# Kernel tuning notes

Measured on AMD Instinct MI355X. Metric: run time of the kernel, lower is better.

## Reference

```python
import jax, jax.numpy as jnp
import numpy as np

B, S, D, H, HG, W, DFF = 2, 4096, 1024, 16, 2, 128, 4096
NEG = -1e30  # stands in for -inf in the original masking (exp underflows to exactly 0)


def _chunk(x, w):
    # overlapping chunks of size 2w with hop w (tf.signal.frame equivalent)
    b, s, d = x.shape
    blocks = x.reshape(b, s // w, w, d)
    return jnp.concatenate([blocks[:, :-1], blocks[:, 1:]], axis=2)  # [b, s//w-1, 2w, d]


def _sliding_scores(q, k, w):
    # q,k: [BH, S, dh] (q pre-scaled). Returns banded scores [BH, S, 2w+1].
    bh, s, d = q.shape
    c = s // w - 1
    attn = jnp.einsum('bcxd,bcyd->bcxy', _chunk(q, w), _chunk(k, w))  # [bh,c,2w,2w]
    # pad one row then reshape: the skew trick from the source (_pad_and_transpose_last_two_dims)
    dca = jnp.pad(attn, ((0, 0), (0, 0), (0, 1), (0, 0))).reshape(bh, c, 2 * w, 2 * w + 1)
    up = jnp.concatenate([dca[:, :, :w, :w + 1], dca[:, -1:, w:, :w + 1]], axis=1)          # [bh,c+1,w,w+1]
    first = jnp.roll(dca, shift=(1, w), axis=(2, 3))[:, :1, :w, :w]                          # first-chunk lower triangle
    low = jnp.concatenate([first, dca[:, :, -(w + 1):-1, w + 1:]], axis=1)                   # [bh,c+1,w,w]
    return jnp.concatenate([low, up], axis=-1).reshape(bh, s, 2 * w + 1)


def _invalid_mask(s, w):
    # _mask_invalid_locations: mask band positions that fall outside [0, S)
    m = jnp.tril(jnp.ones((w, w + 1), jnp.float32))[::-1]
    m = jnp.pad(m, ((0, s - w), (0, w)))
    return (m + m[::-1, ::-1]) > 0  # [s, 2w+1]


def _sliding_value(p, v, w):
    # p: [BH, S, 2w+1] band probs, v: [BH, S, dh] -> [BH, S, dh]
    bh, s, kk = p.shape
    d = v.shape[-1]
    c = s // w
    cp = jnp.pad(p.reshape(bh, c, w, kk), ((0, 0), (0, 0), (0, 0), (0, w + 1)))
    # pad-and-diagonalize skew: row r shifted right by r -> aligns band with 3w value window
    cp = cp.reshape(bh, c, w * (3 * w + 2))[:, :, :-w].reshape(bh, c, w, 3 * w + 1)[:, :, :, :-1]
    pv = jnp.pad(v, ((0, 0), (w, w), (0, 0))).reshape(bh, c + 2, w, d)
    cv = jnp.concatenate([pv[:, :-2], pv[:, 1:-1], pv[:, 2:]], axis=2)  # [bh,c,3w,d]
    return jnp.einsum('bcwk,bckd->bcwd', cp, cv).reshape(bh, s, d)


def _layernorm(x, g, b):
    mu = jnp.mean(x, -1, keepdims=True)
    var = jnp.mean(jnp.square(x - mu), -1, keepdims=True)
    return (x - mu) * jax.lax.rsqrt(var + 1e-6) * g + b


def setup_inputs() -> dict:
    key = jax.random.key(0)
    ks = jax.random.split(key, 8)
    dense = lambda k, i, o: 0.02 * jax.random.normal(k, (i, o), jnp.float32)
    return {
        'x': jax.random.normal(ks[0], (B, S, D), jnp.float32),
        'mask': jnp.zeros((B, 1, 1, S), jnp.float32),
        'wq_k': dense(ks[1], D, D), 'wq_b': jnp.zeros((D,), jnp.float32),
        'wk_k': dense(ks[2], D, D), 'wk_b': jnp.zeros((D,), jnp.float32),
        'wv_k': dense(ks[3], D, D), 'wv_b': jnp.zeros((D,), jnp.float32),
        'wo_k': dense(ks[4], D, D), 'wo_b': jnp.zeros((D,), jnp.float32),
        'ffn_w1': dense(ks[5], D, DFF), 'ffn_b1': jnp.zeros((DFF,), jnp.float32),
        'ffn_w2': dense(ks[6], DFF, D), 'ffn_b2': jnp.zeros((D,), jnp.float32),
        'ln1_g': jnp.ones((D,), jnp.float32), 'ln1_b': jnp.zeros((D,), jnp.float32),
        'ln2_g': jnp.ones((D,), jnp.float32), 'ln2_b': jnp.zeros((D,), jnp.float32),
    }


def reference(x, mask, wq_k, wq_b, wk_k, wk_b, wv_k, wv_b, wo_k, wo_b,
              ffn_w1, ffn_b1, ffn_w2, ffn_b2, ln1_g, ln1_b, ln2_g, ln2_b):
    dh = D // H
    hl = H - HG
    split = lambda t: t.reshape(B, S, H, dh).transpose(0, 2, 1, 3)  # [B,H,S,dh]
    q, k, v = split(x @ wq_k + wq_b), split(x @ wk_k + wk_b), split(x @ wv_k + wv_b)
    scale = 1.0 / jnp.sqrt(jnp.float32(dh))
    # ---- local (sliding-window) heads ----
    ql = (q[:, :hl] * scale).reshape(B * hl, S, dh)
    kl = k[:, :hl].reshape(B * hl, S, dh)
    vl = v[:, :hl].reshape(B * hl, S, dh)
    scores = _sliding_scores(ql, kl, W)
    scores = jnp.where(_invalid_mask(S, W)[None], NEG, scores)
    out_l = _sliding_value(jax.nn.softmax(scores, axis=-1), vl, W).reshape(B, hl, S, dh)
    # ---- global heads (full attention, graph_mask=None branch) ----
    logits = jnp.einsum('bhqd,bhkd->bhqk', q[:, hl:], k[:, hl:]) * scale + mask * (-1000.0)
    out_g = jnp.einsum('bhqk,bhkd->bhqd', jax.nn.softmax(logits, axis=-1), v[:, hl:])
    # ---- merge heads, output proj, residual + LN, FFN (leaky_relu alpha=0.2 = tf default) ----
    attn = jnp.concatenate([out_l, out_g], axis=1).transpose(0, 2, 1, 3).reshape(B, S, D)
    out1 = _layernorm(x + attn @ wo_k + wo_b, ln1_g, ln1_b)
    h = jax.nn.leaky_relu(out1 @ ffn_w1 + ffn_b1, negative_slope=0.2)
    return _layernorm(out1 + h @ ffn_w2 + ffn_b2, ln2_g, ln2_b)
```

## Files before the change

### kernel.cpp

```cpp
#include <hip/hip_runtime.h>
#include <hip/hip_bf16.h>

typedef unsigned short u16;
typedef unsigned int u32;
typedef __attribute__((ext_vector_type(8))) short short8;
typedef __attribute__((ext_vector_type(8))) unsigned short ushort8v;
typedef __attribute__((ext_vector_type(4))) unsigned short ushort4v;
typedef __attribute__((ext_vector_type(4))) float f32x4;

static constexpr int B_ = 2, S_ = 4096, D_ = 1024, H_ = 16, HG_ = 2, W_ = 128, DFF_ = 4096;
static constexpr int HL_ = H_ - HG_;
static constexpr int M_ = B_ * S_;
static constexpr int NCH_ = 4;

static __device__ __forceinline__ u16 f2b(float f) {
    u32 u = __builtin_bit_cast(u32, f);
    u32 r = (u + 0x7fffu + ((u >> 16) & 1u)) >> 16;
    return (u16)r;
}
static __device__ __forceinline__ float b2f(u16 b) {
    return __builtin_bit_cast(float, (u32)b << 16);
}

__global__ __launch_bounds__(256) void k_f32_to_bf16(const float* __restrict__ src,
                                                     u16* __restrict__ dst, int n4) {
    int i = blockIdx.x * 256 + threadIdx.x;
    if (i >= n4) return;
    float4 v = reinterpret_cast<const float4*>(src)[i];
    ushort4v o; o[0] = f2b(v.x); o[1] = f2b(v.y); o[2] = f2b(v.z); o[3] = f2b(v.w);
    reinterpret_cast<ushort4v*>(dst)[i] = o;
}

__global__ __launch_bounds__(256) void k_transpose_bf16(const float* __restrict__ src,
                                                        u16* __restrict__ dst,
                                                        int K, int N, int ro) {
    __shared__ float tile[32][33];
    const int tx = threadIdx.x & 31, ty = threadIdx.x >> 5;
    const int bx = blockIdx.x, by = blockIdx.y;
#pragma unroll
    for (int jj = 0; jj < 4; ++jj) {
        int kk = by * 32 + ty + jj * 8;
        int nn = bx * 32 + tx;
        tile[ty + jj * 8][tx] = src[(size_t)kk * N + nn];
    }
    __syncthreads();
#pragma unroll
    for (int jj = 0; jj < 4; ++jj) {
        int nn = bx * 32 + ty + jj * 8;
        int kk = by * 32 + tx;
        dst[(size_t)(ro + nn) * K + kk] = f2b(tile[tx][ty + jj * 8]);
    }
}

__global__ __launch_bounds__(256) void k_transpose_v(const u16* __restrict__ qkv,
                                                     u16* __restrict__ vT) {
    __shared__ u16 tile[32][33];
    const int tx = threadIdx.x & 31, ty = threadIdx.x >> 5;
    const int s0 = blockIdx.x * 32;
    const int d0 = blockIdx.y * 32;
    const int bh = blockIdx.z;
    const int b = bh >> 4, h = bh & 15;
#pragma unroll
    for (int jj = 0; jj < 4; ++jj) {
        int srow = s0 + ty + jj * 8;
        tile[ty + jj * 8][tx] = qkv[(size_t)(b * S_ + srow) * 3072 + 2048 + h * 64 + d0 + tx];
    }
    __syncthreads();
#pragma unroll
    for (int jj = 0; jj < 4; ++jj) {
        int d = d0 + ty + jj * 8;
        vT[(size_t)((b * H_ + h) * 64 + d) * S_ + s0 + tx] = tile[tx][ty + jj * 8];
    }
}

__global__ void k_pack_bias3(const float* __restrict__ a, const float* __restrict__ b,
                             const float* __restrict__ c, float* __restrict__ dst) {
    int i = blockIdx.x * 256 + threadIdx.x;
    if (i >= 3072) return;
    dst[i] = i < 1024 ? a[i] : (i < 2048 ? b[i - 1024] : c[i - 2048]);
}

#define GLDS16(gp, lp) __builtin_amdgcn_global_load_lds( \
    (const __attribute__((address_space(1))) void*)(gp),  \
    (__attribute__((address_space(3))) void*)(lp), 16, 0, 0)

template <int N>
static __device__ __forceinline__ void vwait() {
    if constexpr (N == 0) asm volatile("s_waitcnt vmcnt(0)" ::: "memory");
    else if constexpr (N == 3) asm volatile("s_waitcnt vmcnt(3)" ::: "memory");
    else asm volatile("s_waitcnt vmcnt(4)" ::: "memory");
    __builtin_amdgcn_sched_barrier(0);
}

template <int BM, bool LEAKY, bool OUTF, bool OUTB>
__global__ __launch_bounds__(512, 2) void k_gemm8(const u16* __restrict__ A, const u16* __restrict__ Bt,
                                                  const float* __restrict__ bias,
                                                  float* __restrict__ Cf, u16* __restrict__ Cb,
                                                  int M, int N, int K) {
    constexpr int MR = BM / 32;
    constexpr int LA = BM / 128;
    constexpr int AHALF = BM * 64;
    constexpr int ABUF = 2 * AHALF;
    constexpr int BHALF = 16384;
    constexpr int PARSZ = ABUF + 2 * BHALF;
    constexpr int NWT = LA + 2;

    __shared__ __align__(16) char smem[2 * PARSZ];

    const int tid = threadIdx.x;
    const int lane = tid & 63, w = tid >> 6;
    const int wm = w >> 2, wn = w & 3;
    const int c = lane & 15, g = lane >> 4;

    const int GX = gridDim.x;
    const int nwg = GX * gridDim.y;
    const int lin = blockIdx.y * GX + blockIdx.x;
    const int qq = nwg >> 3, rm = nwg & 7;
    const int xcd = lin & 7, idx = lin >> 3;
    const int wg = (xcd < rm ? xcd * (qq + 1) : rm * (qq + 1) + (xcd - rm) * qq) + idx;
    const int m0 = (wg % GX) * BM;
    const int n0 = (wg / GX) * 256;

    const int srr = lane >> 2;
    const int sgc = (lane & 3) ^ ((lane >> 4) & 2);
    const u16* gA0 = A + (size_t)(m0 + w * 16 + srr) * K + sgc * 8;
    const u16* gA1 = (LA == 2) ? (A + (size_t)(m0 + 128 + w * 16 + srr) * K + sgc * 8) : gA0;
    const u16* gB0 = Bt + (size_t)(n0 + w * 16 + srr) * K + sgc * 8;
    const u16* gB1 = Bt + (size_t)(n0 + 128 + w * 16 + srr) * K + sgc * 8;

#define STG_A(par, kh, kt) do { \
        char* _d = smem + (par) * PARSZ + (kh) * AHALF + w * 1024; \
        GLDS16(gA0 + (size_t)(kt) * 64 + (kh) * 32, _d); \
        if (LA == 2) GLDS16(gA1 + (size_t)(kt) * 64 + (kh) * 32, _d + 8192); \
    } while (0)
#define STG_B(par, kh, kt) do { \
        char* _d = smem + (par) * PARSZ + ABUF + (kh) * BHALF + w * 1024; \
        GLDS16(gB0 + (size_t)(kt) * 64 + (kh) * 32, _d); \
        GLDS16(gB1 + (size_t)(kt) * 64 + (kh) * 32, _d + 8192); \
    } while (0)

    const int gb = (g ^ ((c >> 3) << 1)) * 16;
    const int arow = c * 64 + gb;

    f32x4 acc[MR][4];
#pragma unroll
    for (int i = 0; i < MR; ++i)
#pragma unroll
        for (int j = 0; j < 4; ++j)
#pragma unroll
            for (int e = 0; e < 4; ++e) acc[i][j][e] = 0.f;

    STG_A(0, 0, 0); STG_B(0, 0, 0); STG_A(0, 1, 0); STG_B(0, 1, 0);
    vwait<0>();
    __builtin_amdgcn_s_barrier();

    const int NK = K >> 6;
    short8 af[MR], b0, b1;
    for (int kt = 0; kt < NK; ++kt) {
        const int par = kt & 1, nxt = par ^ 1;
        const char* bp = smem + par * PARSZ;
        const bool more = (kt + 1) < NK;
#pragma unroll
        for (int mi = 0; mi < MR; ++mi)
            af[mi] = *reinterpret_cast<const short8*>(bp + (wm * MR + mi) * 1024 + arow);
        b0 = *reinterpret_cast<const short8*>(bp + ABUF + (wn * 4 + 0) * 1024 + arow);
        b1 = *reinterpret_cast<const short8*>(bp + ABUF + (wn * 4 + 1) * 1024 + arow);
        if (more) STG_A(nxt, 0, kt + 1);
        __builtin_amdgcn_s_barrier();
        __builtin_amdgcn_s_setprio(1);
#pragma unroll
        for (int mi = 0; mi < MR; ++mi) {
            acc[mi][0] = __builtin_amdgcn_mfma_f32_16x16x32_bf16(af[mi], b0, acc[mi][0], 0, 0, 0);
            acc[mi][1] = __builtin_amdgcn_mfma_f32_16x16x32_bf16(af[mi], b1, acc[mi][1], 0, 0, 0);
        }
        __builtin_amdgcn_s_setprio(0);
        __builtin_amdgcn_s_barrier();
        b0 = *reinterpret_cast<const short8*>(bp + ABUF + (wn * 4 + 2) * 1024 + arow);
        b1 = *reinterpret_cast<const short8*>(bp + ABUF + (wn * 4 + 3) * 1024 + arow);
        if (more) STG_B(nxt, 0, kt + 1);
        __builtin_amdgcn_s_barrier();
        __builtin_amdgcn_s_setprio(1);
#pragma unroll
        for (int mi = 0; mi < MR; ++mi) {
            acc[mi][2] = __builtin_amdgcn_mfma_f32_16x16x32_bf16(af[mi], b0, acc[mi][2], 0, 0, 0);
            acc[mi][3] = __builtin_amdgcn_mfma_f32_16x16x32_bf16(af[mi], b1, acc[mi][3], 0, 0, 0);
        }
        __builtin_amdgcn_s_setprio(0);
        if (more) vwait<NWT>(); else vwait<0>();
        __builtin_amdgcn_s_barrier();
#pragma unroll
        for (int mi = 0; mi < MR; ++mi)
            af[mi] = *reinterpret_cast<const short8*>(bp + AHALF + (wm * MR + mi) * 1024 + arow);
        b0 = *reinterpret_cast<const short8*>(bp + ABUF + BHALF + (wn * 4 + 0) * 1024 + arow);
        b1 = *reinterpret_cast<const short8*>(bp + ABUF + BHALF + (wn * 4 + 1) * 1024 + arow);
        if (more) STG_A(nxt, 1, kt + 1);
        __builtin_amdgcn_s_barrier();
        __builtin_amdgcn_s_setprio(1);
#pragma unroll
        for (int mi = 0; mi < MR; ++mi) {
            acc[mi][0] = __builtin_amdgcn_mfma_f32_16x16x32_bf16(af[mi], b0, acc[mi][0], 0, 0, 0);
            acc[mi][1] = __builtin_amdgcn_mfma_f32_16x16x32_bf16(af[mi], b1, acc[mi][1], 0, 0, 0);
        }
        __builtin_amdgcn_s_setprio(0);
        __builtin_amdgcn_s_barrier();
        b0 = *reinterpret_cast<const short8*>(bp + ABUF + BHALF + (wn * 4 + 2) * 1024 + arow);
        b1 = *reinterpret_cast<const short8*>(bp + ABUF + BHALF + (wn * 4 + 3) * 1024 + arow);
        if (more) STG_B(nxt, 1, kt + 1);
        __builtin_amdgcn_s_barrier();
        __builtin_amdgcn_s_setprio(1);
#pragma unroll
        for (int mi = 0; mi < MR; ++mi) {
            acc[mi][2] = __builtin_amdgcn_mfma_f32_16x16x32_bf16(af[mi], b0, acc[mi][2], 0, 0, 0);
            acc[mi][3] = __builtin_amdgcn_mfma_f32_16x16x32_bf16(af[mi], b1, acc[mi][3], 0, 0, 0);
        }
        __builtin_amdgcn_s_setprio(0);
        if (more) vwait<NWT>();
        __builtin_amdgcn_s_barrier();
    }

#pragma unroll
    for (int mi = 0; mi < MR; ++mi) {
        const int rowb = m0 + wm * (BM / 2) + mi * 16 + g * 4;
#pragma unroll
        for (int ni = 0; ni < 4; ++ni) {
            const int col = n0 + wn * 64 + ni * 16 + c;
            const float bs = bias[col];
#pragma unroll
            for (int j = 0; j < 4; ++j) {
                float v = acc[mi][ni][j] + bs;
                if (LEAKY) v = v > 0.f ? v : 0.2f * v;
                const size_t idxo = (size_t)(rowb + j) * N + col;
                if (OUTF) Cf[idxo] = v;
                if (OUTB) Cb[idxo] = f2b(v);
            }
        }
    }
#undef STG_A
#undef STG_B
}

__global__ __launch_bounds__(256) void k_attn_local(const u16* __restrict__ qkv,
                                                    const u16* __restrict__ vT,
                                                    u16* __restrict__ out) {
    __shared__ __align__(16) u16 Kl[64][72];
    __shared__ __align__(16) u16 Vl[64][72];
    __shared__ __align__(16) u16 Pl[4][1024];
    const int tid = threadIdx.x, lane = tid & 63, wave = tid >> 6;
    const int c = lane & 15, g = lane >> 4;
    const int b = blockIdx.z, h = blockIdx.y;
    const int q0 = blockIdx.x * 64;
    const int qrow = q0 + wave * 16 + c;

    short8 qf[2];
    {
        const u16* qp = qkv + (size_t)(b * S_ + qrow) * 3072 + h * 64 + g * 8;
        qf[0] = *reinterpret_cast<const short8*>(qp);
        qf[1] = *reinterpret_cast<const short8*>(qp + 32);
    }

    f32x4 acc[4];
#pragma unroll
    for (int dt = 0; dt < 4; ++dt)
#pragma unroll
        for (int j = 0; j < 4; ++j) acc[dt][j] = 0.f;
    float mrow = -1e30f, lrow = 0.f;

    const int t_lo = max(0, q0 - W_) >> 6;
    const int t_hi = min(S_ - 1, q0 + 63 + W_) >> 6;
    u16* pw = Pl[wave];

    for (int t = t_lo; t <= t_hi; ++t) {
        __syncthreads();
#pragma unroll
        for (int it = 0; it < 2; ++it) {
            int L = it * 256 + tid;
            int r = L >> 3, cb = (L & 7) * 8;
            *reinterpret_cast<ushort8v*>(&Kl[r][cb]) =
                *reinterpret_cast<const ushort8v*>(&qkv[(size_t)(b * S_ + t * 64 + r) * 3072 + 1024 + h * 64 + cb]);
            *reinterpret_cast<ushort8v*>(&Vl[r][cb]) =
                *reinterpret_cast<const ushort8v*>(&vT[(size_t)((b * H_ + h) * 64 + r) * S_ + t * 64 + cb]);
        }
        __syncthreads();

        f32x4 s[4];
#pragma unroll
        for (int nt = 0; nt < 4; ++nt)
#pragma unroll
            for (int j = 0; j < 4; ++j) s[nt][j] = 0.f;
        __builtin_amdgcn_s_setprio(1);
#pragma unroll
        for (int kc = 0; kc < 2; ++kc) {
#pragma unroll
            for (int nt = 0; nt < 4; ++nt) {
                short8 kf = *reinterpret_cast<const short8*>(&Kl[nt * 16 + c][kc * 32 + g * 8]);
                s[nt] = __builtin_amdgcn_mfma_f32_16x16x32_bf16(kf, qf[kc], s[nt], 0, 0, 0);
            }
        }
        __builtin_amdgcn_s_setprio(0);

        float p[4][4];
        float tmax = -1e30f;
#pragma unroll
        for (int nt = 0; nt < 4; ++nt)
#pragma unroll
            for (int j = 0; j < 4; ++j) {
                float sv = s[nt][j] * 0.125f;
                int key = t * 64 + nt * 16 + 4 * g + j;
                bool val = (key >= qrow - W_) && (key <= qrow + W_);
                sv = val ? sv : -1e30f;
                p[nt][j] = sv;
                tmax = fmaxf(tmax, sv);
            }
        tmax = fmaxf(tmax, __shfl_xor(tmax, 16));
        tmax = fmaxf(tmax, __shfl_xor(tmax, 32));
        float mnew = fmaxf(mrow, tmax);
        float fac = __expf(mrow - mnew);
        mrow = mnew;
        float psum = 0.f;
#pragma unroll
        for (int nt = 0; nt < 4; ++nt)
#pragma unroll
            for (int j = 0; j < 4; ++j) {
                p[nt][j] = __expf(p[nt][j] - mnew);
                psum += p[nt][j];
            }
        lrow = lrow * fac + psum;
#pragma unroll
        for (int dt = 0; dt < 4; ++dt)
#pragma unroll
            for (int j = 0; j < 4; ++j) acc[dt][j] *= fac;

#pragma unroll
        for (int nt = 0; nt < 4; ++nt)
#pragma unroll
            for (int jp = 0; jp < 2; ++jp) {
                u32 pk = (u32)f2b(p[nt][2 * jp]) | ((u32)f2b(p[nt][2 * jp + 1]) << 16);
                int byteoff = (c << 7) + ((nt * 32 + 8 * g + 4 * jp) ^ ((c & 7) << 4));
                *reinterpret_cast<u32*>(reinterpret_cast<char*>(pw) + byteoff) = pk;
            }
        asm volatile("s_waitcnt lgkmcnt(0)" ::: "memory");

        __builtin_amdgcn_s_setprio(1);
#pragma unroll
        for (int h2 = 0; h2 < 2; ++h2) {
            int rb = (c << 7) + ((h2 * 64 + g * 16) ^ ((c & 7) << 4));
            short8 pa = *reinterpret_cast<const short8*>(reinterpret_cast<char*>(pw) + rb);
#pragma unroll
            for (int dt = 0; dt < 4; ++dt) {
                short8 vf = *reinterpret_cast<const short8*>(&Vl[dt * 16 + c][h2 * 32 + g * 8]);
                acc[dt] = __builtin_amdgcn_mfma_f32_16x16x32_bf16(vf, pa, acc[dt], 0, 0, 0);
            }
        }
        __builtin_amdgcn_s_setprio(0);
    }

    float lfull = lrow + __shfl_xor(lrow, 16);
    lfull += __shfl_xor(lfull, 32);
    const float rinv = 1.0f / lfull;

#pragma unroll
    for (int dt = 0; dt < 4; ++dt) {
        u32 w0 = (u32)f2b(acc[dt][0] * rinv) | ((u32)f2b(acc[dt][1] * rinv) << 16);
        u32 w1 = (u32)f2b(acc[dt][2] * rinv) | ((u32)f2b(acc[dt][3] * rinv) << 16);
        uint2 wv; wv.x = w0; wv.y = w1;
        *reinterpret_cast<uint2*>(out + (size_t)(b * S_ + qrow) * 1024 + h * 64 + dt * 16 + 4 * g) = wv;
    }
}

__global__ __launch_bounds__(256) void k_attn_global_part(const u16* __restrict__ qkv,
                                                          const u16* __restrict__ vT,
                                                          const float* __restrict__ mask,
                                                          float* __restrict__ po,
                                                          float* __restrict__ ml) {
    __shared__ __align__(16) u16 Kl[64][72];
    __shared__ __align__(16) u16 Vl[64][72];
    __shared__ __align__(16) u16 Pl[4][1024];
    __shared__ float maskl[64];
    const int tid = threadIdx.x, lane = tid & 63, wave = tid >> 6;
    const int c = lane & 15, g = lane >> 4;
    const int b = blockIdx.z;
    const int hh = blockIdx.y >> 2, ch = blockIdx.y & 3;
    const int h = HL_ + hh;
    const int q0 = blockIdx.x * 64;
    const int qrow = q0 + wave * 16 + c;

    short8 qf[2];
    {
        const u16* qp = qkv + (size_t)(b * S_ + qrow) * 3072 + h * 64 + g * 8;
        qf[0] = *reinterpret_cast<const short8*>(qp);
        qf[1] = *reinterpret_cast<const short8*>(qp + 32);
    }

    f32x4 acc[4];
#pragma unroll
    for (int dt = 0; dt < 4; ++dt)
#pragma unroll
        for (int j = 0; j < 4; ++j) acc[dt][j] = 0.f;
    float mrow = -1e30f, lrow = 0.f;
    u16* pw = Pl[wave];

    const int t_lo = ch * (S_ / 64 / NCH_), t_hi = t_lo + (S_ / 64 / NCH_) - 1;
    for (int t = t_lo; t <= t_hi; ++t) {
        __syncthreads();
#pragma unroll
        for (int it = 0; it < 2; ++it) {
            int L = it * 256 + tid;
            int r = L >> 3, cb = (L & 7) * 8;
            *reinterpret_cast<ushort8v*>(&Kl[r][cb]) =
                *reinterpret_cast<const ushort8v*>(&qkv[(size_t)(b * S_ + t * 64 + r) * 3072 + 1024 + h * 64 + cb]);
            *reinterpret_cast<ushort8v*>(&Vl[r][cb]) =
                *reinterpret_cast<const ushort8v*>(&vT[(size_t)((b * H_ + h) * 64 + r) * S_ + t * 64 + cb]);
        }
        if (tid < 64) maskl[tid] = mask[b * S_ + t * 64 + tid] * (-1000.0f);
        __syncthreads();

        f32x4 s[4];
#pragma unroll
        for (int nt = 0; nt < 4; ++nt)
#pragma unroll
            for (int j = 0; j < 4; ++j) s[nt][j] = 0.f;
        __builtin_amdgcn_s_setprio(1);
#pragma unroll
        for (int kc = 0; kc < 2; ++kc) {
#pragma unroll
            for (int nt = 0; nt < 4; ++nt) {
                short8 kf = *reinterpret_cast<const short8*>(&Kl[nt * 16 + c][kc * 32 + g * 8]);
                s[nt] = __builtin_amdgcn_mfma_f32_16x16x32_bf16(kf, qf[kc], s[nt], 0, 0, 0);
            }
        }
        __builtin_amdgcn_s_setprio(0);

        float p[4][4];
        float tmax = -1e30f;
#pragma unroll
        for (int nt = 0; nt < 4; ++nt)
#pragma unroll
            for (int j = 0; j < 4; ++j) {
                float sv = s[nt][j] * 0.125f + maskl[nt * 16 + 4 * g + j];
                p[nt][j] = sv;
                tmax = fmaxf(tmax, sv);
            }
        tmax = fmaxf(tmax, __shfl_xor(tmax, 16));
        tmax = fmaxf(tmax, __shfl_xor(tmax, 32));
        float mnew = fmaxf(mrow, tmax);
        float fac = __expf(mrow - mnew);
        mrow = mnew;
        float psum = 0.f;
#pragma unroll
        for (int nt = 0; nt < 4; ++nt)
#pragma unroll
            for (int j = 0; j < 4; ++j) {
                p[nt][j] = __expf(p[nt][j] - mnew);
                psum += p[nt][j];
            }
        lrow = lrow * fac + psum;
#pragma unroll
        for (int dt = 0; dt < 4; ++dt)
#pragma unroll
            for (int j = 0; j < 4; ++j) acc[dt][j] *= fac;

#pragma unroll
        for (int nt = 0; nt < 4; ++nt)
#pragma unroll
            for (int jp = 0; jp < 2; ++jp) {
                u32 pk = (u32)f2b(p[nt][2 * jp]) | ((u32)f2b(p[nt][2 * jp + 1]) << 16);
                int byteoff = (c << 7) + ((nt * 32 + 8 * g + 4 * jp) ^ ((c & 7) << 4));
                *reinterpret_cast<u32*>(reinterpret_cast<char*>(pw) + byteoff) = pk;
            }
        asm volatile("s_waitcnt lgkmcnt(0)" ::: "memory");

        __builtin_amdgcn_s_setprio(1);
#pragma unroll
        for (int h2 = 0; h2 < 2; ++h2) {
            int rb = (c << 7) + ((h2 * 64 + g * 16) ^ ((c & 7) << 4));
            short8 pa = *reinterpret_cast<const short8*>(reinterpret_cast<char*>(pw) + rb);
#pragma unroll
            for (int dt = 0; dt < 4; ++dt) {
                short8 vf = *reinterpret_cast<const short8*>(&Vl[dt * 16 + c][h2 * 32 + g * 8]);
                acc[dt] = __builtin_amdgcn_mfma_f32_16x16x32_bf16(vf, pa, acc[dt], 0, 0, 0);
            }
        }
        __builtin_amdgcn_s_setprio(0);
    }

    float lfull = lrow + __shfl_xor(lrow, 16);
    lfull += __shfl_xor(lfull, 32);

    float* po_blk = po + ((((size_t)(b * HG_ + hh) * NCH_ + ch) * (S_ / 64) + blockIdx.x) * 4096);
    const int ql = wave * 16 + c;
#pragma unroll
    for (int dt = 0; dt < 4; ++dt)
        *reinterpret_cast<f32x4*>(po_blk + ql * 64 + dt * 16 + 4 * g) = acc[dt];
    if (g == 0) {
        size_t mb = (((size_t)(b * HG_ + hh) * NCH_ + ch) * S_ + q0 + ql) * 2;
        ml[mb] = mrow;
        ml[mb + 1] = lfull;
    }
}

__global__ __launch_bounds__(256) void k_attn_merge(const float* __restrict__ po,
                                                    const float* __restrict__ ml,
                                                    u16* __restrict__ out) {
    const int qb = blockIdx.x, hh = blockIdx.y, b = blockIdx.z;
    const int t = threadIdx.x;
    const int ql = t >> 2, d0 = (t & 3) * 16;
    const int q = qb * 64 + ql;

    float mv[NCH_], lv[NCH_];
    float M = -1e30f;
#pragma unroll
    for (int ch = 0; ch < NCH_; ++ch) {
        size_t mb = (((size_t)(b * HG_ + hh) * NCH_ + ch) * S_ + q) * 2;
        mv[ch] = ml[mb];
        lv[ch] = ml[mb + 1];
        M = fmaxf(M, mv[ch]);
    }
    float wch[NCH_], L = 0.f;
#pragma unroll
    for (int ch = 0; ch < NCH_; ++ch) {
        wch[ch] = __expf(mv[ch] - M);
        L += wch[ch] * lv[ch];
    }
    const float rL = 1.0f / L;

    float o[16];
#pragma unroll
    for (int i = 0; i < 16; ++i) o[i] = 0.f;
#pragma unroll
    for (int ch = 0; ch < NCH_; ++ch) {
        const float* pb = po + ((((size_t)(b * HG_ + hh) * NCH_ + ch) * (S_ / 64) + qb) * 4096) + ql * 64 + d0;
        const float w = wch[ch];
#pragma unroll
        for (int i = 0; i < 4; ++i) {
            float4 v = reinterpret_cast<const float4*>(pb)[i];
            o[4 * i + 0] += w * v.x; o[4 * i + 1] += w * v.y;
            o[4 * i + 2] += w * v.z; o[4 * i + 3] += w * v.w;
        }
    }
    ushort8v r0, r1;
#pragma unroll
    for (int i = 0; i < 8; ++i) { r0[i] = f2b(o[i] * rL); r1[i] = f2b(o[8 + i] * rL); }
    u16* op = out + (size_t)(b * S_ + q) * 1024 + (HL_ + hh) * 64 + d0;
    *reinterpret_cast<ushort8v*>(op) = r0;
    *reinterpret_cast<ushort8v*>(op + 8) = r1;
}

__global__ __launch_bounds__(256) void k_ln(const float* __restrict__ base, const float* __restrict__ delta,
                                            const float* __restrict__ g, const float* __restrict__ bt,
                                            float* __restrict__ outf, u16* __restrict__ outb) {
    __shared__ float red[8];
    const int row = blockIdx.x, tid = threadIdx.x;
    const int lane = tid & 63, wave = tid >> 6;
    float4 xb = reinterpret_cast<const float4*>(base + (size_t)row * 1024)[tid];
    float4 xd = reinterpret_cast<const float4*>(delta + (size_t)row * 1024)[tid];
    float x0 = xb.x + xd.x, x1 = xb.y + xd.y, x2 = xb.z + xd.z, x3 = xb.w + xd.w;
    float s = x0 + x1 + x2 + x3;
#pragma unroll
    for (int off = 32; off >= 1; off >>= 1) s += __shfl_xor(s, off);
    if (lane == 0) red[wave] = s;
    __syncthreads();
    float mu = (red[0] + red[1] + red[2] + red[3]) * (1.f / 1024.f);
    float d0 = x0 - mu, d1 = x1 - mu, d2 = x2 - mu, d3 = x3 - mu;
    float s2 = d0 * d0 + d1 * d1 + d2 * d2 + d3 * d3;
#pragma unroll
    for (int off = 32; off >= 1; off >>= 1) s2 += __shfl_xor(s2, off);
    if (lane == 0) red[4 + wave] = s2;
    __syncthreads();
    float var = (red[4] + red[5] + red[6] + red[7]) * (1.f / 1024.f);
    float rs = rsqrtf(var + 1e-6f);
    float4 gv = reinterpret_cast<const float4*>(g)[tid];
    float4 bv = reinterpret_cast<const float4*>(bt)[tid];
    float o0 = d0 * rs * gv.x + bv.x;
    float o1 = d1 * rs * gv.y + bv.y;
    float o2 = d2 * rs * gv.z + bv.z;
    float o3 = d3 * rs * gv.w + bv.w;
    if (outf) {
        float4 ov; ov.x = o0; ov.y = o1; ov.z = o2; ov.w = o3;
        reinterpret_cast<float4*>(outf + (size_t)row * 1024)[tid] = ov;
    }
    if (outb) {
        ushort4v ob; ob[0] = f2b(o0); ob[1] = f2b(o1); ob[2] = f2b(o2); ob[3] = f2b(o3);
        reinterpret_cast<ushort4v*>(outb + (size_t)row * 1024)[tid] = ob;
    }
}

extern "C" void kernel_launch(void* const* d_in, const int* in_sizes, int n_in,
                              void* d_out, int out_size, void* d_ws, size_t ws_size,
                              hipStream_t stream) {
    const float* x    = (const float*)d_in[0];
    const float* mask = (const float*)d_in[1];
    const float* wq   = (const float*)d_in[2];
    const float* wq_b = (const float*)d_in[3];
    const float* wk   = (const float*)d_in[4];
    const float* wk_b = (const float*)d_in[5];
    const float* wv   = (const float*)d_in[6];
    const float* wv_b = (const float*)d_in[7];
    const float* wo   = (const float*)d_in[8];
    const float* wo_b = (const float*)d_in[9];
    const float* w1   = (const float*)d_in[10];
    const float* b1   = (const float*)d_in[11];
    const float* w2   = (const float*)d_in[12];
    const float* b2   = (const float*)d_in[13];
    const float* ln1g = (const float*)d_in[14];
    const float* ln1b = (const float*)d_in[15];
    const float* ln2g = (const float*)d_in[16];
    const float* ln2b = (const float*)d_in[17];
    float* out = (float*)d_out;

    char* ws = (char*)d_ws;
    const size_t MB = 1024ull * 1024ull;
    u16*   qkv_b  = (u16*)(ws + 0);
    u16*   h_b    = (u16*)(ws + 0);
    u16*   vTb    = (u16*)(ws + 64 * MB);
    float* ybuf   = (float*)(ws + 64 * MB);
    float* po     = (float*)(ws + 96 * MB);
    float* ml     = (float*)(ws + 113 * MB);
    float* out1   = (float*)(ws + 96 * MB);
    u16*   xb     = (u16*)(ws + 128 * MB);
    u16*   attn_b = (u16*)(ws + 128 * MB);
    u16*   out1_b = (u16*)(ws + 128 * MB);
    u16*   wT     = (u16*)(ws + 144 * MB);
    float* bias3  = (float*)(ws + 152 * MB);

    const dim3 tb(256);
    const dim3 tg(512);

    k_f32_to_bf16<<<(M_ * D_ / 4 + 255) / 256, tb, 0, stream>>>(x, xb, M_ * D_ / 4);
    k_transpose_bf16<<<dim3(32, 32), tb, 0, stream>>>(wq, wT, 1024, 1024, 0);
    k_transpose_bf16<<<dim3(32, 32), tb, 0, stream>>>(wk, wT, 1024, 1024, 1024);
    k_transpose_bf16<<<dim3(32, 32), tb, 0, stream>>>(wv, wT, 1024, 1024, 2048);
    k_pack_bias3<<<12, tb, 0, stream>>>(wq_b, wk_b, wv_b, bias3);
    k_gemm8<256, false, false, true><<<dim3(M_ / 256, 3072 / 256), tg, 0, stream>>>(
        xb, wT, bias3, nullptr, qkv_b, M_, 3072, 1024);
    k_transpose_v<<<dim3(S_ / 32, 2, B_ * H_), tb, 0, stream>>>(qkv_b, vTb);
    k_attn_local<<<dim3(S_ / 64, HL_, B_), tb, 0, stream>>>(qkv_b, vTb, attn_b);
    k_attn_global_part<<<dim3(S_ / 64, HG_ * NCH_, B_), tb, 0, stream>>>(qkv_b, vTb, mask, po, ml);
    k_attn_merge<<<dim3(S_ / 64, HG_, B_), tb, 0, stream>>>(po, ml, attn_b);
    k_transpose_bf16<<<dim3(32, 32), tb, 0, stream>>>(wo, wT, 1024, 1024, 0);
    k_gemm8<128, false, true, false><<<dim3(M_ / 128, 1024 / 256), tg, 0, stream>>>(
        attn_b, wT, wo_b, ybuf, nullptr, M_, 1024, 1024);
    k_ln<<<M_, tb, 0, stream>>>(x, ybuf, ln1g, ln1b, out1, out1_b);
    k_transpose_bf16<<<dim3(128, 32), tb, 0, stream>>>(w1, wT, 1024, 4096, 0);
    k_gemm8<256, true, false, true><<<dim3(M_ / 256, 4096 / 256), tg, 0, stream>>>(
        out1_b, wT, b1, nullptr, h_b, M_, 4096, 1024);
    k_transpose_bf16<<<dim3(32, 128), tb, 0, stream>>>(w2, wT, 4096, 1024, 0);
    k_gemm8<128, false, true, false><<<dim3(M_ / 128, 1024 / 256), tg, 0, stream>>>(
        h_b, wT, b2, ybuf, nullptr, M_, 1024, 4096);
    k_ln<<<M_, tb, 0, stream>>>(out1, ybuf, ln2g, ln2b, out, nullptr);
}
```

Before: 419.0 us.

## Software-pipeline LDS fragment loads ahead of MFMAs in the bf16 GEMM main loop

Restructures the GEMM k-loop so each quarter step issues the LDS fragment loads for the next MFMA group before running the current one, using double-buffered register fragments (af0/af1, bA/bB) and explicit lgkmcnt waits. It also preloads the first fragments before the loop, drops about half of the workgroup barriers, and retunes the vmcnt waits to match the new staging order. The aim is to hide LDS latency behind matrix-core work and cut barrier stalls. The cost is more live registers and tightly hand-counted waits that could break correctness or occupancy at 2 waves per SIMD.

New measurement: 438.0 us. +4.5%, slower.

```diff
diff --git a/kernel.cpp b/kernel.cpp
--- a/kernel.cpp
+++ b/kernel.cpp
@@ -87,8 +87,16 @@
 template <int N>
 static __device__ __forceinline__ void vwait() {
     if constexpr (N == 0) asm volatile("s_waitcnt vmcnt(0)" ::: "memory");
-    else if constexpr (N == 3) asm volatile("s_waitcnt vmcnt(3)" ::: "memory");
-    else asm volatile("s_waitcnt vmcnt(4)" ::: "memory");
+    else if constexpr (N == 1) asm volatile("s_waitcnt vmcnt(1)" ::: "memory");
+    else asm volatile("s_waitcnt vmcnt(2)" ::: "memory");
+    __builtin_amdgcn_sched_barrier(0);
+}
+template <int N>
+static __device__ __forceinline__ void lwait() {
+    if constexpr (N == 0) asm volatile("s_waitcnt lgkmcnt(0)" ::: "memory");
+    else if constexpr (N == 2) asm volatile("s_waitcnt lgkmcnt(2)" ::: "memory");
+    else if constexpr (N == 6) asm volatile("s_waitcnt lgkmcnt(6)" ::: "memory");
+    else asm volatile("s_waitcnt lgkmcnt(10)" ::: "memory");
     __builtin_amdgcn_sched_barrier(0);
 }
 
@@ -103,7 +111,6 @@
     constexpr int ABUF = 2 * AHALF;
     constexpr int BHALF = 16384;
     constexpr int PARSZ = ABUF + 2 * BHALF;
-    constexpr int NWT = LA + 2;
 
     __shared__ __align__(16) char smem[2 * PARSZ];
 
@@ -138,6 +145,7 @@
         GLDS16(gB0 + (size_t)(kt) * 64 + (kh) * 32, _d); \
         GLDS16(gB1 + (size_t)(kt) * 64 + (kh) * 32, _d + 8192); \
     } while (0)
+#define LD8(p) (*reinterpret_cast<const short8*>(p))
 
     const int gb = (g ^ ((c >> 3) << 1)) * 16;
     const int arow = c * 64 + gb;
@@ -149,73 +157,88 @@
         for (int j = 0; j < 4; ++j)
 #pragma unroll
             for (int e = 0; e < 4; ++e) acc[i][j][e] = 0.f;
+
+    short8 af0[MR], af1[MR], bA0, bA1, bB0, bB1;
 
     STG_A(0, 0, 0); STG_B(0, 0, 0); STG_A(0, 1, 0); STG_B(0, 1, 0);
     vwait<0>();
     __builtin_amdgcn_s_barrier();
+#pragma unroll
+    for (int mi = 0; mi < MR; ++mi)
+        af0[mi] = LD8(smem + (wm * MR + mi) * 1024 + arow);
+    bA0 = LD8(smem + ABUF + (wn * 4 + 0) * 1024 + arow);
+    bA1 = LD8(smem + ABUF + (wn * 4 + 1) * 1024 + arow);
 
     const int NK = K >> 6;
-    short8 af[MR], b0, b1;
     for (int kt = 0; kt < NK; ++kt) {
-        const int par = kt & 1, nxt = par ^ 1;
-        const char* bp = smem + par * PARSZ;
+        const int nxt = (kt + 1) & 1;
+        const char* bp = smem + (kt & 1) * PARSZ;
+        const char* np = smem + nxt * PARSZ;
         const bool more = (kt + 1) < NK;
+
+        __builtin_amdgcn_s_barrier();
+        if (more) STG_A(nxt, 0, kt + 1);
+        bB0 = LD8(bp + ABUF + (wn * 4 + 2) * 1024 + arow);
+        bB1 = LD8(bp + ABUF + (wn * 4 + 3) * 1024 + arow);
+        lwait<2>();
+        __builtin_amdgcn_s_setprio(1);
+#pragma unroll
+        for (int mi = 0; mi < MR; ++mi) {
+            acc[mi][0] = __builtin_amdgcn_mfma_f32_16x16x32_bf16(af0[mi], bA0, acc[mi][0], 0, 0, 0);
+            acc[mi][1] = __builtin_amdgcn_mfma_f32_16x16x32_bf16(af0[mi], bA1, acc[mi][1], 0, 0, 0);
+        }
+        __builtin_amdgcn_s_setprio(0);
+
+        if (more) vwait<LA>(); else vwait<0>();
+        __builtin_amdgcn_s_barrier();
+        if (more) STG_B(nxt, 0, kt + 1);
 #pragma unroll
         for (int mi = 0; mi < MR; ++mi)
-            af[mi] = *reinterpret_cast<const short8*>(bp + (wm * MR + mi) * 1024 + arow);
-        b0 = *reinterpret_cast<const short8*>(bp + ABUF + (wn * 4 + 0) * 1024 + arow);
-        b1 = *reinterpret_cast<const short8*>(bp + ABUF + (wn * 4 + 1) * 1024 + arow);
-        if (more) STG_A(nxt, 0, kt + 1);
+            af1[mi] = LD8(bp + AHALF + (wm * MR + mi) * 1024 + arow);
+        bA0 = LD8(bp + ABUF + BHALF + (wn * 4 + 0) * 1024 + arow);
+        bA1 = LD8(bp + ABUF + BHALF + (wn * 4 + 1) * 1024 + arow);
+        lwait<MR + 2>();
+        __builtin_amdgcn_s_setprio(1);
+#pragma unroll
+        for (int mi = 0; mi < MR; ++mi) {
+            acc[mi][2] = __builtin_amdgcn_mfma_f32_16x16x32_bf16(af0[mi], bB0, acc[mi][2], 0, 0, 0);
+            acc[mi][3] = __builtin_amdgcn_mfma_f32_16x16x32_bf16(af0[mi], bB1, acc[mi][3], 0, 0, 0);
+        }
+        __builtin_amdgcn_s_setprio(0);
+
         __builtin_amdgcn_s_barrier();
+        if (more) STG_A(nxt, 1, kt + 1);
+        bB0 = LD8(bp + ABUF + BHALF + (wn * 4 + 2) * 1024 + arow);
+        bB1 = LD8(bp + ABUF + BHALF + (wn * 4 + 3) * 1024 + arow);
+        lwait<2>();
         __builtin_amdgcn_s_setprio(1);
 #pragma unroll
         for (int mi = 0; mi < MR; ++mi) {
-            acc[mi][0] = __builtin_amdgcn_mfma_f32_16x16x32_bf16(af[mi], b0, acc[mi][0], 0, 0, 0);
-            acc[mi][1] = __builtin_amdgcn_mfma_f32_16x16x32_bf16(af[mi], b1, acc[mi][1], 0, 0, 0);
-        }
-        __builtin_amdgcn_s_setprio(0);
+            acc[mi][0] = __builtin_amdgcn_mfma_f32_16x16x32_bf16(af1[mi], bA0, acc[mi][0], 0, 0, 0);
+            acc[mi][1] = __builtin_amdgcn_mfma_f32_16x16x32_bf16(af1[mi], bA1, acc[mi][1], 0, 0, 0);
+        }
+        __builtin_amdgcn_s_setprio(0);
+
+        if (more) vwait<LA>();
         __builtin_amdgcn_s_barrier();
-        b0 = *reinterpret_cast<const short8*>(bp + ABUF + (wn * 4 + 2) * 1024 + arow);
-        b1 = *reinterpret_cast<const short8*>(bp + ABUF + (wn * 4 + 3) * 1024 + arow);
-        if (more) STG_B(nxt, 0, kt + 1);
-        __builtin_amdgcn_s_barrier();
+        if (more) {
+            STG_B(nxt, 1, kt + 1);
+#pragma unroll
+            for (int mi = 0; mi < MR; ++mi)
+                af0[mi] = LD8(np + (wm * MR + mi) * 1024 + arow);
+            bA0 = LD8(np + ABUF + (wn * 4 + 0) * 1024 + arow);
+            bA1 = LD8(np + ABUF + (wn * 4 + 1) * 1024 + arow);
+            lwait<MR + 2>();
+        } else {
+            lwait<0>();
+        }
         __builtin_amdgcn_s_setprio(1);
 #pragma unroll
         for (int mi = 0; mi < MR; ++mi) {
-            acc[mi][2] = __builtin_amdgcn_mfma_f32_16x16x32_bf16(af[mi], b0, acc[mi][2], 0, 0, 0);
-            acc[mi][3] = __builtin_amdgcn_mfma_f32_16x16x32_bf16(af[mi], b1, acc[mi][3], 0, 0, 0);
-        }
-        __builtin_amdgcn_s_setprio(0);
-        if (more) vwait<NWT>(); else vwait<0>();
-        __builtin_amdgcn_s_barrier();
-#pragma unroll
-        for (int mi = 0; mi < MR; ++mi)
-            af[mi] = *reinterpret_cast<const short8*>(bp + AHALF + (wm * MR + mi) * 1024 + arow);
-        b0 = *reinterpret_cast<const short8*>(bp + ABUF + BHALF + (wn * 4 + 0) * 1024 + arow);
-        b1 = *reinterpret_cast<const short8*>(bp + ABUF + BHALF + (wn * 4 + 1) * 1024 + arow);
-        if (more) STG_A(nxt, 1, kt + 1);
-        __builtin_amdgcn_s_barrier();
-        __builtin_amdgcn_s_setprio(1);
-#pragma unroll
-        for (int mi = 0; mi < MR; ++mi) {
-            acc[mi][0] = __builtin_amdgcn_mfma_f32_16x16x32_bf16(af[mi], b0, acc[mi][0], 0, 0, 0);
-            acc[mi][1] = __builtin_amdgcn_mfma_f32_16x16x32_bf16(af[mi], b1, acc[mi][1], 0, 0, 0);
-        }
-        __builtin_amdgcn_s_setprio(0);
-        __builtin_amdgcn_s_barrier();
-        b0 = *reinterpret_cast<const short8*>(bp + ABUF + BHALF + (wn * 4 + 2) * 1024 + arow);
-        b1 = *reinterpret_cast<const short8*>(bp + ABUF + BHALF + (wn * 4 + 3) * 1024 + arow);
-        if (more) STG_B(nxt, 1, kt + 1);
-        __builtin_amdgcn_s_barrier();
-        __builtin_amdgcn_s_setprio(1);
-#pragma unroll
-        for (int mi = 0; mi < MR; ++mi) {
-            acc[mi][2] = __builtin_amdgcn_mfma_f32_16x16x32_bf16(af[mi], b0, acc[mi][2], 0, 0, 0);
-            acc[mi][3] = __builtin_amdgcn_mfma_f32_16x16x32_bf16(af[mi], b1, acc[mi][3], 0, 0, 0);
-        }
-        __builtin_amdgcn_s_setprio(0);
-        if (more) vwait<NWT>();
-        __builtin_amdgcn_s_barrier();
+            acc[mi][2] = __builtin_amdgcn_mfma_f32_16x16x32_bf16(af1[mi], bB0, acc[mi][2], 0, 0, 0);
+            acc[mi][3] = __builtin_amdgcn_mfma_f32_16x16x32_bf16(af1[mi], bB1, acc[mi][3], 0, 0, 0);
+        }
+        __builtin_amdgcn_s_setprio(0);
     }
 
 #pragma unroll
@@ -237,6 +260,7 @@
     }
 #undef STG_A
 #undef STG_B
+#undef LD8
 }
 
 __global__ __launch_bounds__(256) void k_attn_local(const u16* __restrict__ qkv,
```
